# Optimization experiments

Hardware: AMD Instinct MI355X
Metric: run time of the kernel (lower is better)

## Reference

```python
import jax, jax.numpy as jnp
import numpy as np
import math

D_MODEL = 1024
N_HEADS = 16
HEAD_DIM = D_MODEL // N_HEADS
N, S = 8, 4096


def setup_inputs() -> dict:
    key = jax.random.key(0)
    ks = jax.random.split(key, 11)
    s = 1.0 / math.sqrt(D_MODEL)
    return {
        "Q": jax.random.normal(ks[0], (N, 1, D_MODEL), jnp.float32),
        "K": jax.random.normal(ks[1], (N, S, D_MODEL), jnp.float32),
        "V": jax.random.normal(ks[2], (N, S, D_MODEL), jnp.float32),
        "Wq": jax.random.normal(ks[3], (D_MODEL, D_MODEL), jnp.float32) * s,
        "bq": jax.random.normal(ks[4], (D_MODEL,), jnp.float32) * s,
        "Wk": jax.random.normal(ks[5], (D_MODEL, D_MODEL), jnp.float32) * s,
        "bk": jax.random.normal(ks[6], (D_MODEL,), jnp.float32) * s,
        "Wv": jax.random.normal(ks[7], (D_MODEL, D_MODEL), jnp.float32) * s,
        "bv": jax.random.normal(ks[8], (D_MODEL,), jnp.float32) * s,
        "Wo": jax.random.normal(ks[9], (D_MODEL, D_MODEL), jnp.float32) * s,
        "bo": jax.random.normal(ks[10], (D_MODEL,), jnp.float32) * s,
    }


def reference(Q, K, V, Wq, bq, Wk, bk, Wv, bv, Wo, bo):
    n, s_len, d = K.shape
    h, hd = N_HEADS, HEAD_DIM
    # Linear projections (torch Linear: y = x @ W.T + b)
    q = (Q @ Wq.T + bq).reshape(n, 1, h, hd)        # [n,1,h,hd]
    k = (K @ Wk.T + bk).reshape(n, s_len, h, hd)    # [n,s,h,hd]
    v = (V @ Wv.T + bv).reshape(n, s_len, h, hd)
    # scores: einsum('npqk,nqsk->nqsp') with K transposed to [n,h,s,hd]
    scores = jnp.einsum('npqk,nqsk->nqsp', q, k.transpose(0, 2, 1, 3)) / math.sqrt(hd)  # [n,h,s,1]
    # NOTE: faithful to source: softmax over the LAST dim, which has size 1 -> all-ones weights
    attn = jax.nn.softmax(scores, axis=-1)  # [n,h,s,1]
    wv = jnp.einsum('nqsp,nqsk->nqpk', attn, v.transpose(0, 2, 1, 3))  # [n,h,1,hd]
    # combine heads: transpose(-2,-3) -> [n,1,h,hd], then flatten to [n,1,d]
    concat = wv.transpose(0, 2, 1, 3).reshape(-1, 1, d)
    return concat @ Wo.T + bo
```

## Files before the change

kernel.cpp:

```cpp
#include <hip/hip_runtime.h>

#define D_MODEL 1024
#define NB      8
#define SLEN    4096
#define D4      (D_MODEL / 4)
#define GROUPS  128
#define ROWS_PER_GROUP (SLEN / GROUPS)
#define NBLOCKS (NB * GROUPS)

__global__ __launch_bounds__(256) void vsum_partial_kernel(
    const float* __restrict__ V, float4* __restrict__ partials) {
    const int b = blockIdx.x;
    const int t = threadIdx.x;
    const int n = b >> 7;
    const int g = b & (GROUPS - 1);

    const float4* Vb = (const float4*)(V + (size_t)n * SLEN * D_MODEL);
    const size_t base = (size_t)g * ROWS_PER_GROUP * D4 + t;

    float4 acc = make_float4(0.f, 0.f, 0.f, 0.f);
#pragma unroll 8
    for (int r = 0; r < ROWS_PER_GROUP; ++r) {
        float4 x = Vb[base + (size_t)r * D4];
        acc.x += x.x; acc.y += x.y; acc.z += x.z; acc.w += x.w;
    }
    partials[(size_t)b * D4 + t] = acc;
}

__global__ __launch_bounds__(256) void vsum_reduce_kernel(
    const float4* __restrict__ partials, float4* __restrict__ Vsum) {
    const int n = blockIdx.x;
    const int t = threadIdx.x;
    float4 acc = make_float4(0.f, 0.f, 0.f, 0.f);
#pragma unroll 8
    for (int g = 0; g < GROUPS; ++g) {
        float4 x = partials[((size_t)n * GROUPS + g) * D4 + t];
        acc.x += x.x; acc.y += x.y; acc.z += x.z; acc.w += x.w;
    }
    Vsum[(size_t)n * D4 + t] = acc;
}

__global__ __launch_bounds__(256) void gemv8_kernel(
    const float4* __restrict__ X,
    const float*  __restrict__ W,
    const float*  __restrict__ bvec,
    float* __restrict__ Y,
    float bias_scale) {
    const int t    = threadIdx.x;
    const int wv   = t >> 6;
    const int lane = t & 63;
    const int i    = blockIdx.x * 4 + wv;

    const float4* Wr = (const float4*)(W + (size_t)i * D_MODEL);

    float acc[NB];
#pragma unroll
    for (int n = 0; n < NB; ++n) acc[n] = 0.f;

#pragma unroll
    for (int g = lane; g < D4; g += 64) {
        float4 w = Wr[g];
#pragma unroll
        for (int n = 0; n < NB; ++n) {
            float4 x = X[n * D4 + g];
            acc[n] += w.x * x.x + w.y * x.y + w.z * x.z + w.w * x.w;
        }
    }

#pragma unroll
    for (int n = 0; n < NB; ++n) {
        float v = acc[n];
#pragma unroll
        for (int off = 32; off > 0; off >>= 1) v += __shfl_down(v, off);
        if (lane == 0) Y[(size_t)n * D_MODEL + i] = v + bias_scale * bvec[i];
    }
}

extern "C" void kernel_launch(void* const* d_in, const int* in_sizes, int n_in,
                              void* d_out, int out_size, void* d_ws, size_t ws_size,
                              hipStream_t stream) {
    const float* V  = (const float*)d_in[2];
    const float* Wv = (const float*)d_in[7];
    const float* bv = (const float*)d_in[8];
    const float* Wo = (const float*)d_in[9];
    const float* bo = (const float*)d_in[10];
    float* out = (float*)d_out;

    float4* partials = (float4*)d_ws;
    float4* Vsum     = partials + (size_t)NBLOCKS * D4;
    float4* vproj    = Vsum + NB * D4;

    vsum_partial_kernel<<<NBLOCKS, 256, 0, stream>>>(V, partials);
    vsum_reduce_kernel<<<NB, 256, 0, stream>>>(partials, Vsum);
    gemv8_kernel<<<D_MODEL / 4, 256, 0, stream>>>(Vsum, Wv, bv, (float*)vproj,
                                                  (float)SLEN);
    gemv8_kernel<<<D_MODEL / 4, 256, 0, stream>>>(vproj, Wo, bo, out, 1.0f);
}
```

Before: 284.2 us.

## Increase V-sum partial groups, parallelize reduction across column chunks, hoist GEMV weight loads

Doubles the number of row groups in the V column-sum partial kernel so more blocks stream V, and rewrites the reduction kernel to use 64 blocks that split columns and groups with a shuffle plus shared-memory combine instead of 8 blocks looping serially. The GEMV loads all weight vectors up front and unrolls the dot product fully. This targets low parallelism in the reduction and latency in the load loops, at the cost of a larger partials buffer in workspace.

Result: no change. 283.2 us (-0.4%).

```diff
diff --git a/kernel.cpp b/kernel.cpp
--- a/kernel.cpp
+++ b/kernel.cpp
@@ -4,7 +4,7 @@
 #define NB      8
 #define SLEN    4096
 #define D4      (D_MODEL / 4)
-#define GROUPS  128
+#define GROUPS  256
 #define ROWS_PER_GROUP (SLEN / GROUPS)
 #define NBLOCKS (NB * GROUPS)
 
@@ -12,7 +12,7 @@
     const float* __restrict__ V, float4* __restrict__ partials) {
     const int b = blockIdx.x;
     const int t = threadIdx.x;
-    const int n = b >> 7;
+    const int n = b >> 8;
     const int g = b & (GROUPS - 1);
 
     const float4* Vb = (const float4*)(V + (size_t)n * SLEN * D_MODEL);
@@ -29,15 +29,39 @@
 
 __global__ __launch_bounds__(256) void vsum_reduce_kernel(
     const float4* __restrict__ partials, float4* __restrict__ Vsum) {
-    const int n = blockIdx.x;
+    const int b = blockIdx.x;
+    const int n = b >> 3;
+    const int c = b & 7;
     const int t = threadIdx.x;
+    const int col = (c << 5) + (t & 31);
+    const int g0  = t >> 5;
+
+    const float4* P = partials + (size_t)n * GROUPS * D4;
     float4 acc = make_float4(0.f, 0.f, 0.f, 0.f);
 #pragma unroll 8
-    for (int g = 0; g < GROUPS; ++g) {
-        float4 x = partials[((size_t)n * GROUPS + g) * D4 + t];
+    for (int k = 0; k < GROUPS / 8; ++k) {
+        float4 x = P[(size_t)(g0 + (k << 3)) * D4 + col];
         acc.x += x.x; acc.y += x.y; acc.z += x.z; acc.w += x.w;
     }
-    Vsum[(size_t)n * D4 + t] = acc;
+    acc.x += __shfl_xor(acc.x, 32);
+    acc.y += __shfl_xor(acc.y, 32);
+    acc.z += __shfl_xor(acc.z, 32);
+    acc.w += __shfl_xor(acc.w, 32);
+
+    __shared__ float4 red[4][32];
+    const int lane = t & 63;
+    const int wv   = t >> 6;
+    if (lane < 32) red[wv][lane] = acc;
+    __syncthreads();
+    if (t < 32) {
+        float4 a = red[0][t], b2 = red[1][t], c2 = red[2][t], d = red[3][t];
+        float4 r;
+        r.x = a.x + b2.x + c2.x + d.x;
+        r.y = a.y + b2.y + c2.y + d.y;
+        r.z = a.z + b2.z + c2.z + d.z;
+        r.w = a.w + b2.w + c2.w + d.w;
+        Vsum[(size_t)n * D4 + (c << 5) + t] = r;
+    }
 }
 
 __global__ __launch_bounds__(256) void gemv8_kernel(
@@ -53,18 +77,22 @@
 
     const float4* Wr = (const float4*)(W + (size_t)i * D_MODEL);
 
+    const float4 w0 = Wr[lane];
+    const float4 w1 = Wr[lane + 64];
+    const float4 w2 = Wr[lane + 128];
+    const float4 w3 = Wr[lane + 192];
+
     float acc[NB];
 #pragma unroll
-    for (int n = 0; n < NB; ++n) acc[n] = 0.f;
-
-#pragma unroll
-    for (int g = lane; g < D4; g += 64) {
-        float4 w = Wr[g];
-#pragma unroll
-        for (int n = 0; n < NB; ++n) {
-            float4 x = X[n * D4 + g];
-            acc[n] += w.x * x.x + w.y * x.y + w.z * x.z + w.w * x.w;
-        }
+    for (int n = 0; n < NB; ++n) {
+        const float4 x0 = X[n * D4 + lane];
+        const float4 x1 = X[n * D4 + lane + 64];
+        const float4 x2 = X[n * D4 + lane + 128];
+        const float4 x3 = X[n * D4 + lane + 192];
+        acc[n] = w0.x * x0.x + w0.y * x0.y + w0.z * x0.z + w0.w * x0.w
+               + w1.x * x1.x + w1.y * x1.y + w1.z * x1.z + w1.w * x1.w
+               + w2.x * x2.x + w2.y * x2.y + w2.z * x2.z + w2.w * x2.w
+               + w3.x * x3.x + w3.y * x3.y + w3.z * x3.z + w3.w * x3.w;
     }
 
 #pragma unroll
@@ -91,7 +119,7 @@
     float4* vproj    = Vsum + NB * D4;
 
     vsum_partial_kernel<<<NBLOCKS, 256, 0, stream>>>(V, partials);
-    vsum_reduce_kernel<<<NB, 256, 0, stream>>>(partials, Vsum);
+    vsum_reduce_kernel<<<64, 256, 0, stream>>>(partials, Vsum);
     gemv8_kernel<<<D_MODEL / 4, 256, 0, stream>>>(Vsum, Wv, bv, (float*)vproj,
                                                   (float)SLEN);
     gemv8_kernel<<<D_MODEL / 4, 256, 0, stream>>>(vproj, Wo, bo, out, 1.0f);
```
